# Kernel tuning notes

Measured on AMD Instinct MI355X. Metric: run time of the kernel, lower is better.

The kernel has to match this reference:

```python
import jax, jax.numpy as jnp
import numpy as np

NUM_HEADS = 16
HIDDEN = 1024
HEAD_DIM = HIDDEN // NUM_HEADS


def setup_inputs() -> dict:
    key = jax.random.key(0)
    ks = jax.random.split(key, 9)
    B, S, D = 2, 2048, HIDDEN
    s = 1.0 / np.sqrt(D)
    return {
        "x": jax.random.normal(ks[0], (B, S, D), dtype=jnp.float32),
        "Wq": jax.random.normal(ks[1], (D, D), dtype=jnp.float32) * s,
        "bq": jnp.zeros((D,), dtype=jnp.float32),
        "Wk": jax.random.normal(ks[2], (D, D), dtype=jnp.float32) * s,
        "bk": jnp.zeros((D,), dtype=jnp.float32),
        "Wv": jax.random.normal(ks[3], (D, D), dtype=jnp.float32) * s,
        "bv": jnp.zeros((D,), dtype=jnp.float32),
        "Wo": jax.random.normal(ks[4], (D, D), dtype=jnp.float32) * s,
        "bo": jnp.zeros((D,), dtype=jnp.float32),
    }


def reference(x, Wq, bq, Wk, bk, Wv, bv, Wo, bo):
    B, S, D = x.shape
    H, Hd = NUM_HEADS, HEAD_DIM
    # projections -> [B, H, S, Hd]
    def proj(W, b):
        return (x @ W + b).reshape(B, S, H, Hd).transpose(0, 2, 1, 3)
    q = proj(Wq, bq)
    k = proj(Wk, bk)
    v = proj(Wv, bv)
    scores = jnp.einsum('bhqd,bhkd->bhqk', q, k) / jnp.sqrt(jnp.float32(Hd))
    p_attn = jax.nn.softmax(scores, axis=-1)  # dropout = identity (eval)
    ctx = jnp.einsum('bhqk,bhkd->bhqd', p_attn, v)
    attn_mean = jnp.mean(p_attn, axis=1)  # [B, S, S]
    out = ctx.transpose(0, 2, 1, 3).reshape(B, S, D) @ Wo + bo
    return out, attn_mean
```

## Files before the change

### kernel.cpp

```cpp
#include <hip/hip_runtime.h>
#include <math.h>

#define NUM_HEADS 16
#define HEAD_DIM  64
#define HIDDEN    1024
#define BATCH     2
#define SEQ       2048

#define QSCALE 0.1803368801111204f

typedef short bf16x8 __attribute__((ext_vector_type(8)));
typedef short short4v __attribute__((ext_vector_type(4)));
typedef float f32x4 __attribute__((ext_vector_type(4)));

#if __has_builtin(__builtin_amdgcn_exp2f)
#define EXP2F __builtin_amdgcn_exp2f
#else
#define EXP2F exp2f
#endif

#define ACQB(N) do { asm volatile("s_waitcnt vmcnt(" #N ")" ::: "memory"); \
                     __builtin_amdgcn_s_barrier(); } while (0)
#define RELB()  do { asm volatile("s_waitcnt lgkmcnt(0)" ::: "memory");   \
                     __builtin_amdgcn_sched_barrier(0);                    \
                     __builtin_amdgcn_s_barrier(); } while (0)

__device__ __forceinline__ short f2bf(float f) {
    union { float f; unsigned int u; } x; x.f = f;
    unsigned int r = x.u + 0x7fffu + ((x.u >> 16) & 1u);
    return (short)(r >> 16);
}

__device__ __forceinline__ unsigned int pack_bf16_trunc(float lo, float hi) {
    return __builtin_amdgcn_perm(__float_as_uint(hi), __float_as_uint(lo), 0x07060302u);
}

__device__ __forceinline__ void async16(const void* g, void* l) {
    __builtin_amdgcn_global_load_lds(
        (const __attribute__((address_space(1))) void*)g,
        (__attribute__((address_space(3))) void*)l, 16, 0, 0);
}

__global__ __launch_bounds__(256)
void prep_kernel(const float* __restrict__ x,
                 const float* __restrict__ Wq, const float* __restrict__ Wk,
                 const float* __restrict__ Wv, const float* __restrict__ Wo,
                 short* __restrict__ xb, short* __restrict__ Wt4)
{
    __shared__ float t[64][65];
    const int tid = threadIdx.x;
    const int bid = blockIdx.x;
    if (bid < 4096) {
        size_t i = ((size_t)bid * 256 + tid) * 4;
        float4 v = *(const float4*)&x[i];
        short4v o;
        o.x = f2bf(v.x); o.y = f2bf(v.y); o.z = f2bf(v.z); o.w = f2bf(v.w);
        *(short4v*)&xb[i] = o;
        return;
    }
    const int tb = bid - 4096;
    const int z  = tb >> 8;
    const int cx = tb & 15, cy = (tb >> 4) & 15;
    const float* W = (z == 0) ? Wq : (z == 1) ? Wk : (z == 2) ? Wv : Wo;
    short* dst = Wt4 + (size_t)z * HIDDEN * HIDDEN;
    const int c0 = cx * 64;
    const int r0 = cy * 64;
    const int cl = tid & 63, rw = tid >> 6;
    #pragma unroll
    for (int p = 0; p < 16; ++p) {
        int row = p * 4 + rw;
        t[row][cl] = W[(size_t)(r0 + row) * HIDDEN + c0 + cl];
    }
    __syncthreads();
    #pragma unroll
    for (int p = 0; p < 16; ++p) {
        int orow = p * 4 + rw;
        dst[(size_t)(c0 + orow) * HIDDEN + r0 + cl] = f2bf(t[cl][orow]);
    }
}

__global__ __launch_bounds__(256)
void qkv_proj_kernel(const short* __restrict__ xb, const short* __restrict__ Wt4,
                     const float* __restrict__ bq, const float* __restrict__ bk,
                     const float* __restrict__ bv,
                     short* __restrict__ Qb, short* __restrict__ Kb,
                     short* __restrict__ Vt)
{
    __shared__ short ldsA[2][128 * 64];
    __shared__ short ldsB[2][128 * 64];
    const int tid = threadIdx.x;
    const int lane = tid & 63, w = tid >> 6;
    const int l = lane & 15, q = lane >> 4;
    const int lin = blockIdx.y * 8 + blockIdx.x;
    const int cid = (lin & 7) * 32 + (lin >> 3);
    const int n0 = (cid & 7) * 128;
    const int m0 = (cid >> 3) * 128;
    const int z  = blockIdx.z;
    const short* Wt = Wt4 + (size_t)z * HIDDEN * HIDDEN;
    const int wm = (w >> 1) * 64, wn = (w & 1) * 64;
    const int sw = l & 7;

    const short* pa[4]; const short* pb[4]; int ldst[4];
    #pragma unroll
    for (int hh = 0; hh < 4; ++hh) {
        int c = hh * 256 + tid;
        int row = c >> 3;
        int kcg = (c & 7) ^ (row & 7);
        pa[hh] = xb + (size_t)(m0 + row) * HIDDEN + kcg * 8;
        pb[hh] = Wt + (size_t)(n0 + row) * HIDDEN + kcg * 8;
        ldst[hh] = c * 8;
    }

    f32x4 acc[4][4];
    #pragma unroll
    for (int i = 0; i < 4; ++i)
        #pragma unroll
        for (int j = 0; j < 4; ++j)
            acc[i][j] = (f32x4){0.f, 0.f, 0.f, 0.f};

    auto STG = [&](int buf) {
        #pragma unroll
        for (int hh = 0; hh < 4; ++hh) {
            async16(pa[hh], &ldsA[buf][ldst[hh]]);
            async16(pb[hh], &ldsB[buf][ldst[hh]]);
            pa[hh] += 64; pb[hh] += 64;
        }
    };
    auto CMP = [&](int buf) {
        #pragma unroll
        for (int kk = 0; kk < 2; ++kk) {
            const int cc = ((4 * kk + q) ^ sw) * 8;
            bf16x8 af[4], bfr[4];
            #pragma unroll
            for (int i = 0; i < 4; ++i)
                af[i] = *(const bf16x8*)&ldsA[buf][(wm + 16 * i + l) * 64 + cc];
            #pragma unroll
            for (int j = 0; j < 4; ++j)
                bfr[j] = *(const bf16x8*)&ldsB[buf][(wn + 16 * j + l) * 64 + cc];
            __builtin_amdgcn_s_setprio(1);
            #pragma unroll
            for (int i = 0; i < 4; ++i)
                #pragma unroll
                for (int j = 0; j < 4; ++j)
                    acc[i][j] = __builtin_amdgcn_mfma_f32_16x16x32_bf16(
                        af[i], bfr[j], acc[i][j], 0, 0, 0);
            __builtin_amdgcn_s_setprio(0);
        }
    };

    STG(0);
    for (int t = 0; t < 15; ++t) {
        STG((t & 1) ^ 1);
        ACQB(8);
        CMP(t & 1);
        RELB();
    }
    ACQB(0);
    CMP(1);

    const float* bias = (z == 0) ? bq : (z == 1) ? bk : bv;
    const float sc = (z == 0) ? QSCALE : 1.0f;
    if (z < 2) {
        short* Ob = (z == 0) ? Qb : Kb;
        #pragma unroll
        for (int j = 0; j < 4; ++j) {
            int n = n0 + wn + 16 * j + l;
            float bval = bias[n];
            int h = n >> 6, hd = n & 63;
            #pragma unroll
            for (int i = 0; i < 4; ++i) {
                #pragma unroll
                for (int reg = 0; reg < 4; ++reg) {
                    int m = m0 + wm + 16 * i + 4 * q + reg;
                    int b_ = m >> 11, s = m & 2047;
                    Ob[(((size_t)(b_ * NUM_HEADS + h) * SEQ) + s) * HEAD_DIM + hd] =
                        f2bf((acc[i][j][reg] + bval) * sc);
                }
            }
        }
    } else {
        #pragma unroll
        for (int j = 0; j < 4; ++j) {
            int n = n0 + wn + 16 * j + l;
            float bval = bias[n];
            int h = n >> 6, hd = n & 63;
            #pragma unroll
            for (int i = 0; i < 4; ++i) {
                int mb = m0 + wm + 16 * i + 4 * q;
                int b_ = mb >> 11, s = mb & 2047;
                short4v pk;
                #pragma unroll
                for (int reg = 0; reg < 4; ++reg)
                    pk[reg] = f2bf(acc[i][j][reg] + bval);
                *(short4v*)&Vt[(((size_t)(b_ * NUM_HEADS + h) * HEAD_DIM) + hd) * SEQ + s] = pk;
            }
        }
    }
}

__global__ __launch_bounds__(512, 4)
void flash_kernel(const short* __restrict__ Qb, const short* __restrict__ Kb,
                  const short* __restrict__ Vt, short* __restrict__ Cb,
                  float* __restrict__ Lb)
{
    __shared__ __align__(16) char fsm[35840];
    short (*Ks)[64 * 64] = (short (*)[64 * 64])fsm;
    short (*Vs)[64 * 64] = (short (*)[64 * 64])(fsm + 16384);
    float (*Xch)[64][35] = (float (*)[64][35])fsm;

    const int tid = threadIdx.x, lane = tid & 63, w = tid >> 6;
    const int l = lane & 15, q = lane >> 4;
    const int qg = w & 3;
    const int kh = w >> 2;
    const int q0 = blockIdx.x * 128;
    const int Q0 = q0 + qg * 32;
    const int h = blockIdx.y, b = blockIdx.z;
    const size_t base  = (size_t)(b * NUM_HEADS + h) * SEQ * HEAD_DIM;
    const size_t vbase = (size_t)(b * NUM_HEADS + h) * HEAD_DIM * SEQ;

    bf16x8 bq[2][2];
    #pragma unroll
    for (int u = 0; u < 2; ++u)
        #pragma unroll
        for (int ks = 0; ks < 2; ++ks)
            bq[u][ks] = *(const bf16x8*)(Qb + base +
                (size_t)(Q0 + 16 * u + l) * HEAD_DIM + 32 * ks + 8 * q);

    const int c = tid;
    const int row = c >> 3;
    const int g = ((c & 7) ^ (row & 7)) * 8;
    const short* kp = Kb + base + (size_t)row * HEAD_DIM + g;
    const short* vp = Vt + vbase + (size_t)row * SEQ + g;

    const int sw = l & 7;
    int kaddr[2];
    #pragma unroll
    for (int ks = 0; ks < 2; ++ks)
        kaddr[ks] = (32 * kh + l) * 64 + ((4 * ks + q) ^ sw) * 8;
    const int vc0 = 4 * kh + (q >> 1);
    const int vaddr0 = l * 64 + ((vc0      ^ sw) * 8) + 4 * (q & 1);
    const int vaddr1 = l * 64 + (((vc0 + 2) ^ sw) * 8) + 4 * (q & 1);

    f32x4 ctx[2][4];
    #pragma unroll
    for (int u = 0; u < 2; ++u)
        #pragma unroll
        for (int m = 0; m < 4; ++m) ctx[u][m] = (f32x4){0.f, 0.f, 0.f, 0.f};
    float l_part[2] = {0.f, 0.f};

    auto STG = [&](int buf) {
        async16(kp, &Ks[buf][c * 8]);
        async16(vp, &Vs[buf][c * 8]);
        kp += 64 * HEAD_DIM;
        vp += 64;
    };
    auto CMP = [&](int buf) {
        f32x4 st[2][2];
        #pragma unroll
        for (int u = 0; u < 2; ++u)
            #pragma unroll
            for (int t = 0; t < 2; ++t) st[u][t] = (f32x4){0.f, 0.f, 0.f, 0.f};
        __builtin_amdgcn_s_setprio(1);
        #pragma unroll
        for (int ks = 0; ks < 2; ++ks) {
            #pragma unroll
            for (int t = 0; t < 2; ++t) {
                bf16x8 ak = *(const bf16x8*)&Ks[buf][kaddr[ks] + t * 1024];
                st[0][t] = __builtin_amdgcn_mfma_f32_16x16x32_bf16(ak, bq[0][ks], st[0][t], 0, 0, 0);
                st[1][t] = __builtin_amdgcn_mfma_f32_16x16x32_bf16(ak, bq[1][ks], st[1][t], 0, 0, 0);
            }
        }
        __builtin_amdgcn_s_setprio(0);
        union { unsigned int u32[4]; bf16x8 v; } bp[2];
        #pragma unroll
        for (int u = 0; u < 2; ++u) {
            #pragma unroll
            for (int t = 0; t < 2; ++t) {
                float p0 = EXP2F(st[u][t][0]);
                float p1 = EXP2F(st[u][t][1]);
                float p2 = EXP2F(st[u][t][2]);
                float p3 = EXP2F(st[u][t][3]);
                l_part[u] += (p0 + p1) + (p2 + p3);
                bp[u].u32[2 * t]     = pack_bf16_trunc(p0, p1);
                bp[u].u32[2 * t + 1] = pack_bf16_trunc(p2, p3);
            }
        }
        __builtin_amdgcn_s_setprio(1);
        #pragma unroll
        for (int m = 0; m < 4; ++m) {
            short4v g0 = *(const short4v*)&Vs[buf][vaddr0 + m * 1024];
            short4v g1 = *(const short4v*)&Vs[buf][vaddr1 + m * 1024];
            bf16x8 av = __builtin_shufflevector(g0, g1, 0, 1, 2, 3, 4, 5, 6, 7);
            ctx[0][m] = __builtin_amdgcn_mfma_f32_16x16x32_bf16(av, bp[0].v, ctx[0][m], 0, 0, 0);
            ctx[1][m] = __builtin_amdgcn_mfma_f32_16x16x32_bf16(av, bp[1].v, ctx[1][m], 0, 0, 0);
        }
        __builtin_amdgcn_s_setprio(0);
    };

    STG(0); STG(1);
    ACQB(2);
    for (int tp = 0; tp < 15; ++tp) {
        CMP(0); RELB(); STG(0); ACQB(2);
        CMP(1); RELB(); STG(1); ACQB(2);
    }
    CMP(0); RELB(); ACQB(0);
    CMP(1);

    __syncthreads();

    if (kh == 1) {
        float* dst = &Xch[qg][lane][0];
        #pragma unroll
        for (int u = 0; u < 2; ++u)
            #pragma unroll
            for (int m = 0; m < 4; ++m)
                #pragma unroll
                for (int r = 0; r < 4; ++r)
                    dst[u * 16 + m * 4 + r] = ctx[u][m][r];
        dst[32] = l_part[0];
        dst[33] = l_part[1];
    }
    __syncthreads();
    if (kh == 0) {
        const float* src = &Xch[qg][lane][0];
        #pragma unroll
        for (int u = 0; u < 2; ++u)
            #pragma unroll
            for (int m = 0; m < 4; ++m)
                #pragma unroll
                for (int r = 0; r < 4; ++r)
                    ctx[u][m][r] += src[u * 16 + m * 4 + r];

        #pragma unroll
        for (int u = 0; u < 2; ++u) {
            float rs = l_part[u] + src[32 + u];
            rs += __shfl_xor(rs, 16);
            rs += __shfl_xor(rs, 32);
            float inv_l = 1.0f / rs;
            int s = Q0 + 16 * u + l;
            #pragma unroll
            for (int t = 0; t < 4; ++t) {
                short4v pk;
                #pragma unroll
                for (int reg = 0; reg < 4; ++reg)
                    pk[reg] = f2bf(ctx[u][t][reg] * inv_l);
                *(short4v*)&Cb[(((size_t)(b * NUM_HEADS + h) * SEQ) + s) * HEAD_DIM + 16 * t + 4 * q] = pk;
            }
            if (q == 0)
                Lb[(size_t)(b * NUM_HEADS + h) * SEQ + s] = inv_l;
        }
    }
}

__global__ __launch_bounds__(256)
void tail_kernel(const short* __restrict__ Cb, const short* __restrict__ Wot,
                 const float* __restrict__ bo, float* __restrict__ out,
                 const short* __restrict__ Qb, const short* __restrict__ Kb,
                 const float* __restrict__ Lb, float* __restrict__ amean)
{
    __shared__ short smem[24576];
    const int tid = threadIdx.x, lane = tid & 63, w = tid >> 6;
    const int l = lane & 15, q = lane >> 4;
    const int sw = l & 7;
    const int bid = blockIdx.x;
    const int r3 = bid % 3, g3 = bid / 3;

    if (r3 == 2) {
        short (*ldsA)[64 * 64]  = (short (*)[64 * 64])smem;
        short (*ldsB)[128 * 64] = (short (*)[128 * 64])(smem + 8192);
        const int cid = (g3 & 7) * 64 + (g3 >> 3);
        const int n0 = (cid & 7) * 128;
        const int m0 = (cid >> 3) * 64;

        const short* pa[2]; const short* pb[4]; int lda[2], ldb[4];
        #pragma unroll
        for (int hh = 0; hh < 2; ++hh) {
            int cc = hh * 256 + tid;
            int rowc = cc >> 3;
            int kcg = (cc & 7) ^ (rowc & 7);
            int m = m0 + rowc;
            int b_ = m >> 11, s = m & 2047;
            pa[hh] = Cb + (((size_t)(b_ * NUM_HEADS) * SEQ) + s) * HEAD_DIM + kcg * 8;
            lda[hh] = cc * 8;
        }
        #pragma unroll
        for (int hh = 0; hh < 4; ++hh) {
            int cc = hh * 256 + tid;
            int rowc = cc >> 3;
            int kcg = (cc & 7) ^ (rowc & 7);
            pb[hh] = Wot + (size_t)(n0 + rowc) * HIDDEN + kcg * 8;
            ldb[hh] = cc * 8;
        }

        f32x4 acc[4][2];
        #pragma unroll
        for (int i = 0; i < 4; ++i)
            #pragma unroll
            for (int j = 0; j < 2; ++j)
                acc[i][j] = (f32x4){0.f, 0.f, 0.f, 0.f};

        auto STG = [&](int buf) {
            #pragma unroll
            for (int hh = 0; hh < 2; ++hh) {
                async16(pa[hh], &ldsA[buf][lda[hh]]);
                pa[hh] += (size_t)SEQ * HEAD_DIM;
            }
            #pragma unroll
            for (int hh = 0; hh < 4; ++hh) {
                async16(pb[hh], &ldsB[buf][ldb[hh]]);
                pb[hh] += 64;
            }
        };
        auto CMP = [&](int buf) {
            #pragma unroll
            for (int kk = 0; kk < 2; ++kk) {
                const int cc = ((4 * kk + q) ^ sw) * 8;
                bf16x8 af[4], bfr[2];
                #pragma unroll
                for (int i = 0; i < 4; ++i)
                    af[i] = *(const bf16x8*)&ldsA[buf][(16 * i + l) * 64 + cc];
                #pragma unroll
                for (int j = 0; j < 2; ++j)
                    bfr[j] = *(const bf16x8*)&ldsB[buf][(32 * w + 16 * j + l) * 64 + cc];
                __builtin_amdgcn_s_setprio(1);
                #pragma unroll
                for (int i = 0; i < 4; ++i)
                    #pragma unroll
                    for (int j = 0; j < 2; ++j)
                        acc[i][j] = __builtin_amdgcn_mfma_f32_16x16x32_bf16(
                            af[i], bfr[j], acc[i][j], 0, 0, 0);
                __builtin_amdgcn_s_setprio(0);
            }
        };

        STG(0);
        for (int t = 0; t < 15; ++t) {
            STG((t & 1) ^ 1);
            ACQB(6);
            CMP(t & 1);
            RELB();
        }
        ACQB(0);
        CMP(1);

        #pragma unroll
        for (int j = 0; j < 2; ++j) {
            int n = n0 + 32 * w + 16 * j + l;
            float bval = bo[n];
            #pragma unroll
            for (int i = 0; i < 4; ++i)
                #pragma unroll
                for (int reg = 0; reg < 4; ++reg) {
                    int m = m0 + 16 * i + 4 * q + reg;
                    out[(size_t)m * HIDDEN + n] = acc[i][j][reg] + bval;
                }
        }
    } else {
        short (*Qs)[64 * 64]  = (short (*)[64 * 64])smem;
        short (*Ks)[128 * 64] = (short (*)[128 * 64])(smem + 8192);
        const int a  = g3 * 2 + r3;
        const int k0 = (a & 15) * 128;
        const int qy = (a >> 4) & 31;
        const int q0 = qy * 64;
        const int b  = a >> 9;
        const size_t HSTRIDE = (size_t)SEQ * HEAD_DIM;

        const short* qp[2];
        const short* kp[4];
        {
            const size_t base0 = (size_t)(b * NUM_HEADS) * HSTRIDE;
            #pragma unroll
            for (int i = 0; i < 2; ++i) {
                int cc = 256 * i + tid;
                int rowc = cc >> 3;
                int gg = ((cc & 7) ^ (rowc & 7)) * 8;
                qp[i] = Qb + base0 + (size_t)(q0 + rowc) * HEAD_DIM + gg;
            }
            #pragma unroll
            for (int i = 0; i < 4; ++i) {
                int cc = 256 * i + tid;
                int rowc = cc >> 3;
                int gg = ((cc & 7) ^ (rowc & 7)) * 8;
                kp[i] = Kb + base0 + (size_t)(k0 + rowc) * HEAD_DIM + gg;
            }
        }

        f32x4 macc[2][4];
        #pragma unroll
        for (int tk = 0; tk < 2; ++tk)
            #pragma unroll
            for (int tq = 0; tq < 4; ++tq)
                macc[tk][tq] = (f32x4){0.f, 0.f, 0.f, 0.f};

        auto STG = [&](int buf) {
            #pragma unroll
            for (int i = 0; i < 2; ++i) { async16(qp[i], &Qs[buf][(256 * i + tid) * 8]); qp[i] += HSTRIDE; }
            #pragma unroll
            for (int i = 0; i < 4; ++i) { async16(kp[i], &Ks[buf][(256 * i + tid) * 8]); kp[i] += HSTRIDE; }
        };
        int hc = 0;
        auto CMP = [&](int buf) {
            int h = hc++;
            float linv[4];
            #pragma unroll
            for (int tq = 0; tq < 4; ++tq)
                linv[tq] = Lb[(size_t)(b * NUM_HEADS + h) * SEQ + q0 + 16 * tq + l];

            bf16x8 bq[4][2];
            #pragma unroll
            for (int tq = 0; tq < 4; ++tq)
                #pragma unroll
                for (int ks = 0; ks < 2; ++ks) {
                    int cc = (4 * ks + q) ^ sw;
                    bq[tq][ks] = *(const bf16x8*)&Qs[buf][((16 * tq + l) * 8 + cc) * 8];
                }
            #pragma unroll
            for (int tk = 0; tk < 2; ++tk) {
                bf16x8 ak[2];
                #pragma unroll
                for (int ks = 0; ks < 2; ++ks) {
                    int cc = (4 * ks + q) ^ sw;
                    ak[ks] = *(const bf16x8*)&Ks[buf][((32 * w + 16 * tk + l) * 8 + cc) * 8];
                }
                #pragma unroll
                for (int tq = 0; tq < 4; ++tq) {
                    f32x4 st = (f32x4){0.f, 0.f, 0.f, 0.f};
                    st = __builtin_amdgcn_mfma_f32_16x16x32_bf16(ak[0], bq[tq][0], st, 0, 0, 0);
                    st = __builtin_amdgcn_mfma_f32_16x16x32_bf16(ak[1], bq[tq][1], st, 0, 0, 0);
                    float li = linv[tq];
                    #pragma unroll
                    for (int reg = 0; reg < 4; ++reg)
                        macc[tk][tq][reg] += EXP2F(st[reg]) * li;
                }
            }
        };

        STG(0); STG(1);
        ACQB(6);
        for (int tp = 0; tp < 7; ++tp) {
            CMP(0); RELB(); STG(0); ACQB(6);
            CMP(1); RELB(); STG(1); ACQB(6);
        }
        CMP(0); RELB(); ACQB(0);
        CMP(1);

        const float inv_h = 1.0f / (float)NUM_HEADS;
        #pragma unroll
        for (int tq = 0; tq < 4; ++tq) {
            int row_q = q0 + 16 * tq + l;
            #pragma unroll
            for (int tk = 0; tk < 2; ++tk) {
                int col_k = k0 + 32 * w + 16 * tk + 4 * q;
                f32x4 o;
                #pragma unroll
                for (int reg = 0; reg < 4; ++reg) o[reg] = macc[tk][tq][reg] * inv_h;
                *(f32x4*)&amean[((size_t)b * SEQ + row_q) * SEQ + col_k] = o;
            }
        }
    }
}

extern "C" void kernel_launch(void* const* d_in, const int* in_sizes, int n_in,
                              void* d_out, int out_size, void* d_ws, size_t ws_size,
                              hipStream_t stream)
{
    const float* x  = (const float*)d_in[0];
    const float* Wq = (const float*)d_in[1];
    const float* bq = (const float*)d_in[2];
    const float* Wk = (const float*)d_in[3];
    const float* bk = (const float*)d_in[4];
    const float* Wv = (const float*)d_in[5];
    const float* bv = (const float*)d_in[6];
    const float* Wo = (const float*)d_in[7];
    const float* bo = (const float*)d_in[8];

    float* out   = (float*)d_out;
    float* amean = out + (size_t)BATCH * SEQ * HIDDEN;

    const size_t NELEM = (size_t)BATCH * NUM_HEADS * SEQ * HEAD_DIM;
    short* ws  = (short*)d_ws;
    short* xb  = ws;
    short* Wt4 = xb + NELEM;
    short* Qb  = Wt4 + 4 * (size_t)HIDDEN * HIDDEN;
    short* Kb  = Qb + NELEM;
    short* Vt  = Kb + NELEM;
    short* Cb  = Vt + NELEM;
    float* Lb  = (float*)(Cb + NELEM);

    dim3 blk(256);
    prep_kernel<<<dim3(4096 + 1024), blk, 0, stream>>>(x, Wq, Wk, Wv, Wo, xb, Wt4);
    qkv_proj_kernel<<<dim3(8, 32, 3), blk, 0, stream>>>(xb, Wt4, bq, bk, bv, Qb, Kb, Vt);
    flash_kernel<<<dim3(SEQ / 128, NUM_HEADS, BATCH), dim3(512), 0, stream>>>(Qb, Kb, Vt, Cb, Lb);
    tail_kernel<<<dim3(1536), blk, 0, stream>>>(Cb, Wt4 + 3 * (size_t)HIDDEN * HIDDEN, bo, out,
                                                Qb, Kb, Lb, amean);
}
```

Baseline: 230.8 us.

## Replace LDS double buffering with single buffer and register-staged fragments

The QKV projection, output projection and attention-mean loops switch from double-buffered LDS staging to a single LDS buffer. Each step loads all MFMA fragments into registers, releases LDS, issues the next async global-to-LDS copy and then runs the MFMAs while that copy is in flight. This halves LDS use per block so more blocks can be resident, at the cost of more live registers and a full vmcnt(0) wait each iteration instead of partial waits.

```diff
diff --git a/kernel.cpp b/kernel.cpp
--- a/kernel.cpp
+++ b/kernel.cpp
@@ -86,8 +86,8 @@
                      short* __restrict__ Qb, short* __restrict__ Kb,
                      short* __restrict__ Vt)
 {
-    __shared__ short ldsA[2][128 * 64];
-    __shared__ short ldsB[2][128 * 64];
+    __shared__ short ldsA[128 * 64];
+    __shared__ short ldsB[128 * 64];
     const int tid = threadIdx.x;
     const int lane = tid & 63, w = tid >> 6;
     const int l = lane & 15, q = lane >> 4;
@@ -118,45 +118,43 @@
         for (int j = 0; j < 4; ++j)
             acc[i][j] = (f32x4){0.f, 0.f, 0.f, 0.f};
 
-    auto STG = [&](int buf) {
+    auto STG = [&]() {
         #pragma unroll
         for (int hh = 0; hh < 4; ++hh) {
-            async16(pa[hh], &ldsA[buf][ldst[hh]]);
-            async16(pb[hh], &ldsB[buf][ldst[hh]]);
+            async16(pa[hh], &ldsA[ldst[hh]]);
+            async16(pb[hh], &ldsB[ldst[hh]]);
             pa[hh] += 64; pb[hh] += 64;
         }
     };
-    auto CMP = [&](int buf) {
+
+    STG();
+    ACQB(0);
+    for (int t = 0; t < 16; ++t) {
+        bf16x8 af[4][2], bfr[4][2];
         #pragma unroll
         for (int kk = 0; kk < 2; ++kk) {
             const int cc = ((4 * kk + q) ^ sw) * 8;
-            bf16x8 af[4], bfr[4];
             #pragma unroll
             for (int i = 0; i < 4; ++i)
-                af[i] = *(const bf16x8*)&ldsA[buf][(wm + 16 * i + l) * 64 + cc];
+                af[i][kk] = *(const bf16x8*)&ldsA[(wm + 16 * i + l) * 64 + cc];
             #pragma unroll
             for (int j = 0; j < 4; ++j)
-                bfr[j] = *(const bf16x8*)&ldsB[buf][(wn + 16 * j + l) * 64 + cc];
-            __builtin_amdgcn_s_setprio(1);
+                bfr[j][kk] = *(const bf16x8*)&ldsB[(wn + 16 * j + l) * 64 + cc];
+        }
+        RELB();
+        if (t < 15) STG();
+        __builtin_amdgcn_s_setprio(1);
+        #pragma unroll
+        for (int kk = 0; kk < 2; ++kk)
             #pragma unroll
             for (int i = 0; i < 4; ++i)
                 #pragma unroll
                 for (int j = 0; j < 4; ++j)
                     acc[i][j] = __builtin_amdgcn_mfma_f32_16x16x32_bf16(
-                        af[i], bfr[j], acc[i][j], 0, 0, 0);
-            __builtin_amdgcn_s_setprio(0);
-        }
-    };
-
-    STG(0);
-    for (int t = 0; t < 15; ++t) {
-        STG((t & 1) ^ 1);
-        ACQB(8);
-        CMP(t & 1);
-        RELB();
-    }
-    ACQB(0);
-    CMP(1);
+                        af[i][kk], bfr[j][kk], acc[i][j], 0, 0, 0);
+        __builtin_amdgcn_s_setprio(0);
+        if (t < 15) ACQB(0);
+    }
 
     const float* bias = (z == 0) ? bq : (z == 1) ? bk : bv;
     const float sc = (z == 0) ? QSCALE : 1.0f;
@@ -358,7 +356,7 @@
                  const short* __restrict__ Qb, const short* __restrict__ Kb,
                  const float* __restrict__ Lb, float* __restrict__ amean)
 {
-    __shared__ short smem[24576];
+    __shared__ __align__(16) short smem[12288];
     const int tid = threadIdx.x, lane = tid & 63, w = tid >> 6;
     const int l = lane & 15, q = lane >> 4;
     const int sw = l & 7;
@@ -366,8 +364,8 @@
     const int r3 = bid % 3, g3 = bid / 3;
 
     if (r3 == 2) {
-        short (*ldsA)[64 * 64]  = (short (*)[64 * 64])smem;
-        short (*ldsB)[128 * 64] = (short (*)[128 * 64])(smem + 8192);
+        short* ldsA = smem;
+        short* ldsB = smem + 4096;
         const int cid = (g3 & 7) * 64 + (g3 >> 3);
         const int n0 = (cid & 7) * 128;
         const int m0 = (cid >> 3) * 64;
@@ -399,49 +397,47 @@
             for (int j = 0; j < 2; ++j)
                 acc[i][j] = (f32x4){0.f, 0.f, 0.f, 0.f};
 
-        auto STG = [&](int buf) {
+        auto STG = [&]() {
             #pragma unroll
             for (int hh = 0; hh < 2; ++hh) {
-                async16(pa[hh], &ldsA[buf][lda[hh]]);
+                async16(pa[hh], &ldsA[lda[hh]]);
                 pa[hh] += (size_t)SEQ * HEAD_DIM;
             }
             #pragma unroll
             for (int hh = 0; hh < 4; ++hh) {
-                async16(pb[hh], &ldsB[buf][ldb[hh]]);
+                async16(pb[hh], &ldsB[ldb[hh]]);
                 pb[hh] += 64;
             }
         };
-        auto CMP = [&](int buf) {
+
+        STG();
+        ACQB(0);
+        for (int t = 0; t < 16; ++t) {
+            bf16x8 af[4][2], bfr[2][2];
             #pragma unroll
             for (int kk = 0; kk < 2; ++kk) {
                 const int cc = ((4 * kk + q) ^ sw) * 8;
-                bf16x8 af[4], bfr[2];
                 #pragma unroll
                 for (int i = 0; i < 4; ++i)
-                    af[i] = *(const bf16x8*)&ldsA[buf][(16 * i + l) * 64 + cc];
+                    af[i][kk] = *(const bf16x8*)&ldsA[(16 * i + l) * 64 + cc];
                 #pragma unroll
                 for (int j = 0; j < 2; ++j)
-                    bfr[j] = *(const bf16x8*)&ldsB[buf][(32 * w + 16 * j + l) * 64 + cc];
-                __builtin_amdgcn_s_setprio(1);
+                    bfr[j][kk] = *(const bf16x8*)&ldsB[(32 * w + 16 * j + l) * 64 + cc];
+            }
+            RELB();
+            if (t < 15) STG();
+            __builtin_amdgcn_s_setprio(1);
+            #pragma unroll
+            for (int kk = 0; kk < 2; ++kk)
                 #pragma unroll
                 for (int i = 0; i < 4; ++i)
                     #pragma unroll
                     for (int j = 0; j < 2; ++j)
                         acc[i][j] = __builtin_amdgcn_mfma_f32_16x16x32_bf16(
-                            af[i], bfr[j], acc[i][j], 0, 0, 0);
-                __builtin_amdgcn_s_setprio(0);
-            }
-        };
-
-        STG(0);
-        for (int t = 0; t < 15; ++t) {
-            STG((t & 1) ^ 1);
-            ACQB(6);
-            CMP(t & 1);
-            RELB();
-        }
-        ACQB(0);
-        CMP(1);
+                            af[i][kk], bfr[j][kk], acc[i][j], 0, 0, 0);
+            __builtin_amdgcn_s_setprio(0);
+            if (t < 15) ACQB(0);
+        }
 
         #pragma unroll
         for (int j = 0; j < 2; ++j) {
@@ -456,8 +452,8 @@
                 }
         }
     } else {
-        short (*Qs)[64 * 64]  = (short (*)[64 * 64])smem;
-        short (*Ks)[128 * 64] = (short (*)[128 * 64])(smem + 8192);
+        short* Qs = smem;
+        short* Ks = smem + 4096;
         const int a  = g3 * 2 + r3;
         const int k0 = (a & 15) * 128;
         const int qy = (a >> 4) & 31;
@@ -492,57 +488,49 @@
             for (int tq = 0; tq < 4; ++tq)
                 macc[tk][tq] = (f32x4){0.f, 0.f, 0.f, 0.f};
 
-        auto STG = [&](int buf) {
-            #pragma unroll
-            for (int i = 0; i < 2; ++i) { async16(qp[i], &Qs[buf][(256 * i + tid) * 8]); qp[i] += HSTRIDE; }
-            #pragma unroll
-            for (int i = 0; i < 4; ++i) { async16(kp[i], &Ks[buf][(256 * i + tid) * 8]); kp[i] += HSTRIDE; }
+        auto STG = [&]() {
+            #pragma unroll
+            for (int i = 0; i < 2; ++i) { async16(qp[i], &Qs[(256 * i + tid) * 8]); qp[i] += HSTRIDE; }
+            #pragma unroll
+            for (int i = 0; i < 4; ++i) { async16(kp[i], &Ks[(256 * i + tid) * 8]); kp[i] += HSTRIDE; }
         };
-        int hc = 0;
-        auto CMP = [&](int buf) {
-            int h = hc++;
+
+        STG();
+        ACQB(0);
+        for (int h = 0; h < 16; ++h) {
             float linv[4];
             #pragma unroll
             for (int tq = 0; tq < 4; ++tq)
                 linv[tq] = Lb[(size_t)(b * NUM_HEADS + h) * SEQ + q0 + 16 * tq + l];
 
-            bf16x8 bq[4][2];
-            #pragma unroll
-            for (int tq = 0; tq < 4; ++tq)
-                #pragma unroll
-                for (int ks = 0; ks < 2; ++ks) {
-                    int cc = (4 * ks + q) ^ sw;
-                    bq[tq][ks] = *(const bf16x8*)&Qs[buf][((16 * tq + l) * 8 + cc) * 8];
-                }
+            bf16x8 bq[4][2], ak[2][2];
+            #pragma unroll
+            for (int ks = 0; ks < 2; ++ks) {
+                const int cc = ((4 * ks + q) ^ sw) * 8;
+                #pragma unroll
+                for (int tq = 0; tq < 4; ++tq)
+                    bq[tq][ks] = *(const bf16x8*)&Qs[(16 * tq + l) * 64 + cc];
+                #pragma unroll
+                for (int tk = 0; tk < 2; ++tk)
+                    ak[tk][ks] = *(const bf16x8*)&Ks[(32 * w + 16 * tk + l) * 64 + cc];
+            }
+            RELB();
+            if (h < 15) STG();
             #pragma unroll
             for (int tk = 0; tk < 2; ++tk) {
-                bf16x8 ak[2];
-                #pragma unroll
-                for (int ks = 0; ks < 2; ++ks) {
-                    int cc = (4 * ks + q) ^ sw;
-                    ak[ks] = *(const bf16x8*)&Ks[buf][((32 * w + 16 * tk + l) * 8 + cc) * 8];
-                }
                 #pragma unroll
                 for (int tq = 0; tq < 4; ++tq) {
                     f32x4 st = (f32x4){0.f, 0.f, 0.f, 0.f};
-                    st = __builtin_amdgcn_mfma_f32_16x16x32_bf16(ak[0], bq[tq][0], st, 0, 0, 0);
-                    st = __builtin_amdgcn_mfma_f32_16x16x32_bf16(ak[1], bq[tq][1], st, 0, 0, 0);
+                    st = __builtin_amdgcn_mfma_f32_16x16x32_bf16(ak[tk][0], bq[tq][0], st, 0, 0, 0);
+                    st = __builtin_amdgcn_mfma_f32_16x16x32_bf16(ak[tk][1], bq[tq][1], st, 0, 0, 0);
                     float li = linv[tq];
                     #pragma unroll
                     for (int reg = 0; reg < 4; ++reg)
                         macc[tk][tq][reg] += EXP2F(st[reg]) * li;
                 }
             }
-        };
-
-        STG(0); STG(1);
-        ACQB(6);
-        for (int tp = 0; tp < 7; ++tp) {
-            CMP(0); RELB(); STG(0); ACQB(6);
-            CMP(1); RELB(); STG(1); ACQB(6);
-        }
-        CMP(0); RELB(); ACQB(0);
-        CMP(1);
+            if (h < 15) ACQB(0);
+        }
 
         const float inv_h = 1.0f / (float)NUM_HEADS;
         #pragma unroll
```

After: 229.9 us. Within noise of the previous version (-0.4%).

## Remap flash and tail blocks per XCD and single-buffer QKV projection LDS

Applied to the files above, without the earlier changes.

Flash and tail kernels switch to a 1D grid whose block index is decoded so that blocks sharing a head, or sharing Wo columns and K ranges, land on the same XCD (bid & 7). The aim is more L2 reuse of K/V and weight tiles. The QKV projection GEMM moves from double-buffered to single-buffered LDS: it reads all fragments into registers, releases the buffer, then issues the next load during the MFMAs. This halves LDS use, which may allow more resident blocks, but exposes load latency behind a full barrier each iteration.

```diff
diff --git a/kernel.cpp b/kernel.cpp
--- a/kernel.cpp
+++ b/kernel.cpp
@@ -86,8 +86,8 @@
                      short* __restrict__ Qb, short* __restrict__ Kb,
                      short* __restrict__ Vt)
 {
-    __shared__ short ldsA[2][128 * 64];
-    __shared__ short ldsB[2][128 * 64];
+    __shared__ short ldsA[128 * 64];
+    __shared__ short ldsB[128 * 64];
     const int tid = threadIdx.x;
     const int lane = tid & 63, w = tid >> 6;
     const int l = lane & 15, q = lane >> 4;
@@ -118,45 +118,43 @@
         for (int j = 0; j < 4; ++j)
             acc[i][j] = (f32x4){0.f, 0.f, 0.f, 0.f};
 
-    auto STG = [&](int buf) {
+    auto STG = [&]() {
         #pragma unroll
         for (int hh = 0; hh < 4; ++hh) {
-            async16(pa[hh], &ldsA[buf][ldst[hh]]);
-            async16(pb[hh], &ldsB[buf][ldst[hh]]);
+            async16(pa[hh], &ldsA[ldst[hh]]);
+            async16(pb[hh], &ldsB[ldst[hh]]);
             pa[hh] += 64; pb[hh] += 64;
         }
     };
-    auto CMP = [&](int buf) {
+
+    STG();
+    ACQB(0);
+    for (int t = 0; t < 16; ++t) {
+        bf16x8 af[4][2], bfr[4][2];
         #pragma unroll
         for (int kk = 0; kk < 2; ++kk) {
             const int cc = ((4 * kk + q) ^ sw) * 8;
-            bf16x8 af[4], bfr[4];
             #pragma unroll
             for (int i = 0; i < 4; ++i)
-                af[i] = *(const bf16x8*)&ldsA[buf][(wm + 16 * i + l) * 64 + cc];
+                af[i][kk] = *(const bf16x8*)&ldsA[(wm + 16 * i + l) * 64 + cc];
             #pragma unroll
             for (int j = 0; j < 4; ++j)
-                bfr[j] = *(const bf16x8*)&ldsB[buf][(wn + 16 * j + l) * 64 + cc];
-            __builtin_amdgcn_s_setprio(1);
+                bfr[j][kk] = *(const bf16x8*)&ldsB[(wn + 16 * j + l) * 64 + cc];
+        }
+        RELB();
+        if (t < 15) STG();
+        __builtin_amdgcn_s_setprio(1);
+        #pragma unroll
+        for (int kk = 0; kk < 2; ++kk)
             #pragma unroll
             for (int i = 0; i < 4; ++i)
                 #pragma unroll
                 for (int j = 0; j < 4; ++j)
                     acc[i][j] = __builtin_amdgcn_mfma_f32_16x16x32_bf16(
-                        af[i], bfr[j], acc[i][j], 0, 0, 0);
-            __builtin_amdgcn_s_setprio(0);
-        }
-    };
-
-    STG(0);
-    for (int t = 0; t < 15; ++t) {
-        STG((t & 1) ^ 1);
-        ACQB(8);
-        CMP(t & 1);
-        RELB();
-    }
-    ACQB(0);
-    CMP(1);
+                        af[i][kk], bfr[j][kk], acc[i][j], 0, 0, 0);
+        __builtin_amdgcn_s_setprio(0);
+        if (t < 15) ACQB(0);
+    }
 
     const float* bias = (z == 0) ? bq : (z == 1) ? bk : bv;
     const float sc = (z == 0) ? QSCALE : 1.0f;
@@ -212,9 +210,12 @@
     const int l = lane & 15, q = lane >> 4;
     const int qg = w & 3;
     const int kh = w >> 2;
-    const int q0 = blockIdx.x * 128;
+    const int bid = blockIdx.x;
+    const int xcd = bid & 7, j = bid >> 3;
+    const int h  = xcd + 8 * (j & 1);
+    const int b  = (j >> 1) & 1;
+    const int q0 = (j >> 2) * 128;
     const int Q0 = q0 + qg * 32;
-    const int h = blockIdx.y, b = blockIdx.z;
     const size_t base  = (size_t)(b * NUM_HEADS + h) * SEQ * HEAD_DIM;
     const size_t vbase = (size_t)(b * NUM_HEADS + h) * HEAD_DIM * SEQ;
 
@@ -358,19 +359,19 @@
                  const short* __restrict__ Qb, const short* __restrict__ Kb,
                  const float* __restrict__ Lb, float* __restrict__ amean)
 {
-    __shared__ short smem[24576];
+    __shared__ __align__(16) short smem[24576];
     const int tid = threadIdx.x, lane = tid & 63, w = tid >> 6;
     const int l = lane & 15, q = lane >> 4;
     const int sw = l & 7;
     const int bid = blockIdx.x;
-    const int r3 = bid % 3, g3 = bid / 3;
+    const int xcd = bid & 7, j = bid >> 3;
+    const int r3 = j % 3, j3 = j / 3;
 
     if (r3 == 2) {
         short (*ldsA)[64 * 64]  = (short (*)[64 * 64])smem;
         short (*ldsB)[128 * 64] = (short (*)[128 * 64])(smem + 8192);
-        const int cid = (g3 & 7) * 64 + (g3 >> 3);
-        const int n0 = (cid & 7) * 128;
-        const int m0 = (cid >> 3) * 64;
+        const int n0 = xcd * 128;
+        const int m0 = j3 * 64;
 
         const short* pa[2]; const short* pb[4]; int lda[2], ldb[4];
         #pragma unroll
@@ -396,8 +397,8 @@
         #pragma unroll
         for (int i = 0; i < 4; ++i)
             #pragma unroll
-            for (int j = 0; j < 2; ++j)
-                acc[i][j] = (f32x4){0.f, 0.f, 0.f, 0.f};
+            for (int jj = 0; jj < 2; ++jj)
+                acc[i][jj] = (f32x4){0.f, 0.f, 0.f, 0.f};
 
         auto STG = [&](int buf) {
             #pragma unroll
@@ -420,15 +421,15 @@
                 for (int i = 0; i < 4; ++i)
                     af[i] = *(const bf16x8*)&ldsA[buf][(16 * i + l) * 64 + cc];
                 #pragma unroll
-                for (int j = 0; j < 2; ++j)
-                    bfr[j] = *(const bf16x8*)&ldsB[buf][(32 * w + 16 * j + l) * 64 + cc];
+                for (int jj = 0; jj < 2; ++jj)
+                    bfr[jj] = *(const bf16x8*)&ldsB[buf][(32 * w + 16 * jj + l) * 64 + cc];
                 __builtin_amdgcn_s_setprio(1);
                 #pragma unroll
                 for (int i = 0; i < 4; ++i)
                     #pragma unroll
-                    for (int j = 0; j < 2; ++j)
-                        acc[i][j] = __builtin_amdgcn_mfma_f32_16x16x32_bf16(
-                            af[i], bfr[j], acc[i][j], 0, 0, 0);
+                    for (int jj = 0; jj < 2; ++jj)
+                        acc[i][jj] = __builtin_amdgcn_mfma_f32_16x16x32_bf16(
+                            af[i], bfr[jj], acc[i][jj], 0, 0, 0);
                 __builtin_amdgcn_s_setprio(0);
             }
         };
@@ -444,25 +445,23 @@
         CMP(1);
 
         #pragma unroll
-        for (int j = 0; j < 2; ++j) {
-            int n = n0 + 32 * w + 16 * j + l;
+        for (int jj = 0; jj < 2; ++jj) {
+            int n = n0 + 32 * w + 16 * jj + l;
             float bval = bo[n];
             #pragma unroll
             for (int i = 0; i < 4; ++i)
                 #pragma unroll
                 for (int reg = 0; reg < 4; ++reg) {
                     int m = m0 + 16 * i + 4 * q + reg;
-                    out[(size_t)m * HIDDEN + n] = acc[i][j][reg] + bval;
+                    out[(size_t)m * HIDDEN + n] = acc[i][jj][reg] + bval;
                 }
         }
     } else {
         short (*Qs)[64 * 64]  = (short (*)[64 * 64])smem;
         short (*Ks)[128 * 64] = (short (*)[128 * 64])(smem + 8192);
-        const int a  = g3 * 2 + r3;
-        const int k0 = (a & 15) * 128;
-        const int qy = (a >> 4) & 31;
-        const int q0 = qy * 64;
-        const int b  = a >> 9;
+        const int k0 = xcd * 256 + r3 * 128;
+        const int b  = j3 & 1;
+        const int q0 = (j3 >> 1) * 64;
         const size_t HSTRIDE = (size_t)SEQ * HEAD_DIM;
 
         const short* qp[2];
@@ -506,27 +505,24 @@
             for (int tq = 0; tq < 4; ++tq)
                 linv[tq] = Lb[(size_t)(b * NUM_HEADS + h) * SEQ + q0 + 16 * tq + l];
 
-            bf16x8 bq[4][2];
-            #pragma unroll
-            for (int tq = 0; tq < 4; ++tq)
-                #pragma unroll
-                for (int ks = 0; ks < 2; ++ks) {
-                    int cc = (4 * ks + q) ^ sw;
-                    bq[tq][ks] = *(const bf16x8*)&Qs[buf][((16 * tq + l) * 8 + cc) * 8];
-                }
+            bf16x8 bq[4][2], ak[2][2];
+            #pragma unroll
+            for (int ks = 0; ks < 2; ++ks) {
+                const int cc = ((4 * ks + q) ^ sw) * 8;
+                #pragma unroll
+                for (int tq = 0; tq < 4; ++tq)
+                    bq[tq][ks] = *(const bf16x8*)&Qs[buf][(16 * tq + l) * 64 + cc];
+                #pragma unroll
+                for (int tk = 0; tk < 2; ++tk)
+                    ak[tk][ks] = *(const bf16x8*)&Ks[buf][(32 * w + 16 * tk + l) * 64 + cc];
+            }
             #pragma unroll
             for (int tk = 0; tk < 2; ++tk) {
-                bf16x8 ak[2];
-                #pragma unroll
-                for (int ks = 0; ks < 2; ++ks) {
-                    int cc = (4 * ks + q) ^ sw;
-                    ak[ks] = *(const bf16x8*)&Ks[buf][((32 * w + 16 * tk + l) * 8 + cc) * 8];
-                }
                 #pragma unroll
                 for (int tq = 0; tq < 4; ++tq) {
                     f32x4 st = (f32x4){0.f, 0.f, 0.f, 0.f};
-                    st = __builtin_amdgcn_mfma_f32_16x16x32_bf16(ak[0], bq[tq][0], st, 0, 0, 0);
-                    st = __builtin_amdgcn_mfma_f32_16x16x32_bf16(ak[1], bq[tq][1], st, 0, 0, 0);
+                    st = __builtin_amdgcn_mfma_f32_16x16x32_bf16(ak[tk][0], bq[tq][0], st, 0, 0, 0);
+                    st = __builtin_amdgcn_mfma_f32_16x16x32_bf16(ak[tk][1], bq[tq][1], st, 0, 0, 0);
                     float li = linv[tq];
                     #pragma unroll
                     for (int reg = 0; reg < 4; ++reg)
@@ -590,7 +586,7 @@
     dim3 blk(256);
     prep_kernel<<<dim3(4096 + 1024), blk, 0, stream>>>(x, Wq, Wk, Wv, Wo, xb, Wt4);
     qkv_proj_kernel<<<dim3(8, 32, 3), blk, 0, stream>>>(xb, Wt4, bq, bk, bv, Qb, Kb, Vt);
-    flash_kernel<<<dim3(SEQ / 128, NUM_HEADS, BATCH), dim3(512), 0, stream>>>(Qb, Kb, Vt, Cb, Lb);
+    flash_kernel<<<dim3(512), dim3(512), 0, stream>>>(Qb, Kb, Vt, Cb, Lb);
     tail_kernel<<<dim3(1536), blk, 0, stream>>>(Cb, Wt4 + 3 * (size_t)HIDDEN * HIDDEN, bo, out,
                                                 Qb, Kb, Lb, amean);
 }
```

Result: no change. 232.8 us (+0.9%).
